# Performance work log

Hardware: AMD Instinct MI355X
Metric: run time of the kernel (lower is better)

The kernel has to match this reference:

```python
import jax, jax.numpy as jnp
import numpy as np
import math

B, S, H = 2, 2048, 2048
NH, NKV, HD = 16, 4, 128


def _rope_tables(seq_len, head_dim):
    # Standard RoPE: freqs over half dim, duplicated to full head_dim.
    inv_freq = 1.0 / (10000.0 ** (np.arange(0, head_dim, 2, dtype=np.float32) / head_dim))
    t = np.arange(seq_len, dtype=np.float32)
    freqs = np.outer(t, inv_freq)  # [S, HD/2]
    emb = np.concatenate([freqs, freqs], axis=-1)  # [S, HD]
    return jnp.asarray(np.cos(emb)), jnp.asarray(np.sin(emb))


def setup_inputs() -> dict:
    key = jax.random.key(0)
    k1, k2, k3, k4 = jax.random.split(key, 4)
    cos, sin = _rope_tables(S, HD)
    return {
        "x": jax.random.normal(k1, (B, S, H), dtype=jnp.float32),
        "cos": cos,
        "sin": sin,
        "Wq": jax.random.normal(k2, (H, NH * HD), dtype=jnp.float32) * (1.0 / math.sqrt(H)),
        "Wkv": jax.random.normal(k3, (H, 2 * NKV * HD), dtype=jnp.float32) * (1.0 / math.sqrt(H)),
        "Wo": jax.random.normal(k4, (NH * HD, H), dtype=jnp.float32) * (1.0 / math.sqrt(NH * HD)),
    }


def _rotate_half(x):
    x1, x2 = jnp.split(x, 2, axis=-1)
    return jnp.concatenate([-x2, x1], axis=-1)


def _apply_rotary(x, cos, sin):
    # x: [B, S, nheads, HD]; cos/sin: [S, HD]
    c = cos[None, :, None, :]
    s = sin[None, :, None, :]
    return x * c + _rotate_half(x) * s


def reference(x, cos, sin, Wq, Wkv, Wo):
    b, s, _ = x.shape
    q = (x @ Wq).reshape(b, s, NH, HD)
    kv = x @ Wkv
    k, v = jnp.split(kv, [NKV * HD], axis=-1)
    k = k.reshape(b, s, NKV, HD)
    v = v.reshape(b, s, NKV, HD)
    q = _apply_rotary(q, cos, sin)
    k = _apply_rotary(k, cos, sin)
    # to [B, heads, S, HD]
    q = jnp.transpose(q, (0, 2, 1, 3))
    k = jnp.transpose(k, (0, 2, 1, 3))
    v = jnp.transpose(v, (0, 2, 1, 3))
    # GQA: repeat K/V heads
    rep = NH // NKV
    k = jnp.repeat(k, rep, axis=1)
    v = jnp.repeat(v, rep, axis=1)
    scale = jnp.asarray(1.0 / math.sqrt(HD), dtype=x.dtype)
    scores = jnp.einsum('bhqd,bhkd->bhqk', q * scale, k)  # [B, NH, S, S]
    causal = jnp.tril(jnp.ones((s, s), dtype=jnp.bool_))
    scores = jnp.where(causal, scores, jnp.asarray(-jnp.inf, scores.dtype))
    attn = jax.nn.softmax(scores, axis=-1)
    out = jnp.einsum('bhqk,bhkd->bhqd', attn, v)
    out = jnp.transpose(out, (0, 2, 1, 3)).reshape(b, s, NH * HD)
    return out @ Wo
```

## Files before the change

### kernel.cpp

```cpp
#include <hip/hip_runtime.h>
#include <math.h>

#define NB 2
#define SEQ 2048
#define HDIM 2048
#define NHD 16
#define NKVH 4
#define HEADD 128
#define MROWS (NB*SEQ)
#define NQCOLS (NHD*HEADD)
#define QKVCOLS 3072

typedef unsigned short ushortT;
typedef __attribute__((ext_vector_type(8))) short short8;
typedef __attribute__((ext_vector_type(4))) float floatx4;
typedef __attribute__((ext_vector_type(4))) unsigned short ushort4v;

__device__ __forceinline__ ushortT f2bf(float f) {
  union { float f; unsigned int u; } v; v.f = f;
  unsigned int r = v.u + 0x7FFFu + ((v.u >> 16) & 1u);
  return (ushortT)(r >> 16);
}
__device__ __forceinline__ float bf2f(ushortT u) {
  union { unsigned int u; float f; } v; v.u = ((unsigned int)u) << 16;
  return v.f;
}

__device__ __forceinline__ void gload16(const ushortT* g, ushortT* l) {
  __builtin_amdgcn_global_load_lds(
      (const __attribute__((address_space(1))) void*)g,
      (__attribute__((address_space(3))) void*)l, 16, 0, 0);
}

__global__ __launch_bounds__(256) void cast_bf16_kernel(
    const float* __restrict__ in, ushortT* __restrict__ out, int n4) {
  int i = blockIdx.x * 256 + threadIdx.x;
  if (i >= n4) return;
  float4 v = ((const float4*)in)[i];
  ushort4v o;
  o.x = f2bf(v.x); o.y = f2bf(v.y); o.z = f2bf(v.z); o.w = f2bf(v.w);
  ((ushort4v*)out)[i] = o;
}

__global__ __launch_bounds__(256) void transpose_cast_kernel(
    const float* __restrict__ in, ushortT* __restrict__ out, int R, int C) {
  __shared__ ushortT tile[32][33];
  int c0 = blockIdx.x * 32, r0 = blockIdx.y * 32;
  int tx = threadIdx.x & 31, ty = threadIdx.x >> 5;
#pragma unroll
  for (int i = 0; i < 4; ++i)
    tile[ty + i*8][tx] = f2bf(in[(size_t)(r0 + ty + i*8) * C + c0 + tx]);
  __syncthreads();
#pragma unroll
  for (int i = 0; i < 4; ++i)
    out[(size_t)(c0 + ty + i*8) * R + r0 + tx] = tile[tx][ty + i*8];
}

__global__ __launch_bounds__(256) void gemm_bt_kernel(
    const ushortT* __restrict__ A, const ushortT* __restrict__ Bt,
    void* __restrict__ C, int M, int N, int K, int c_fp32) {
  __shared__ __align__(16) ushortT lA[128 * 64];
  __shared__ __align__(16) ushortT lB[128 * 64];
  const int m0 = blockIdx.y * 128;
  const int n0 = blockIdx.x * 128;
  const int tid = threadIdx.x;
  const int wave = tid >> 6, lane = tid & 63;
  const int g = lane >> 4, l15 = lane & 15;
  const int wm = (wave >> 1) * 64, wn = (wave & 1) * 64;
  const int sw = l15 & 7;

  floatx4 acc[4][4] = {};

  for (int kt = 0; kt < K; kt += 64) {
    __syncthreads();
#pragma unroll
    for (int i = 0; i < 4; ++i) {
      int s = i * 256 + tid;
      int r = s >> 3, j = s & 7;
      int col8 = j ^ (r & 7);
      gload16(A  + (size_t)(m0 + r) * K + kt + col8 * 8, lA + s * 8);
      gload16(Bt + (size_t)(n0 + r) * K + kt + col8 * 8, lB + s * 8);
    }
    __syncthreads();
#pragma unroll
    for (int ks = 0; ks < 2; ++ks) {
      short8 af[4], bfv[4];
#pragma unroll
      for (int t = 0; t < 4; ++t) {
        af[t]  = *(const short8*)(lA + (wm + t * 16 + l15) * 64 + ((ks * 4 + g) ^ sw) * 8);
        bfv[t] = *(const short8*)(lB + (wn + t * 16 + l15) * 64 + ((ks * 4 + g) ^ sw) * 8);
      }
#pragma unroll
      for (int mt = 0; mt < 4; ++mt)
#pragma unroll
        for (int nt = 0; nt < 4; ++nt)
          acc[mt][nt] = __builtin_amdgcn_mfma_f32_16x16x32_bf16(
              af[mt], bfv[nt], acc[mt][nt], 0, 0, 0);
    }
  }

#pragma unroll
  for (int mt = 0; mt < 4; ++mt)
#pragma unroll
    for (int nt = 0; nt < 4; ++nt)
#pragma unroll
      for (int r = 0; r < 4; ++r) {
        int row = m0 + wm + mt * 16 + g * 4 + r;
        int col = n0 + wn + nt * 16 + l15;
        float v = acc[mt][nt][r];
        if (c_fp32) ((float*)C)[(size_t)row * N + col] = v;
        else ((ushortT*)C)[(size_t)row * N + col] = f2bf(v);
      }
}

__global__ __launch_bounds__(256) void rope_q_kernel(
    const ushortT* __restrict__ QKVtmp, const float* __restrict__ cosT,
    const float* __restrict__ sinT, ushortT* __restrict__ Qr) {
  int idx = blockIdx.x * 256 + threadIdx.x;
  int d = idx & 63;
  int t = idx >> 6;
  int h = t & (NHD - 1);
  int bs = t >> 4;
  int s = bs & (SEQ - 1);
  int b = bs >> 11;
  float c = cosT[s * HEADD + d], sn = sinT[s * HEADD + d];
  float q1 = bf2f(QKVtmp[(size_t)bs * QKVCOLS + h * HEADD + d]);
  float q2 = bf2f(QKVtmp[(size_t)bs * QKVCOLS + h * HEADD + d + 64]);
  size_t o = ((size_t)(b * NHD + h) * SEQ + s) * HEADD + d;
  Qr[o]      = f2bf(q1 * c - q2 * sn);
  Qr[o + 64] = f2bf(q2 * c + q1 * sn);
}

__global__ __launch_bounds__(256) void rope_k_kernel(
    const ushortT* __restrict__ QKVtmp, const float* __restrict__ cosT,
    const float* __restrict__ sinT, ushortT* __restrict__ Kr) {
  int idx = blockIdx.x * 256 + threadIdx.x;
  int d = idx & 63;
  int t = idx >> 6;
  int kvh = t & (NKVH - 1);
  int bs = t >> 2;
  int s = bs & (SEQ - 1);
  int b = bs >> 11;
  float c = cosT[s * HEADD + d], sn = sinT[s * HEADD + d];
  float k1 = bf2f(QKVtmp[(size_t)bs * QKVCOLS + 2048 + kvh * HEADD + d]);
  float k2 = bf2f(QKVtmp[(size_t)bs * QKVCOLS + 2048 + kvh * HEADD + d + 64]);
  size_t o = ((size_t)(b * NKVH + kvh) * SEQ + s) * HEADD + d;
  Kr[o]      = f2bf(k1 * c - k2 * sn);
  Kr[o + 64] = f2bf(k2 * c + k1 * sn);
}

__global__ __launch_bounds__(256) void v_relayout_kernel(
    const ushortT* __restrict__ QKVtmp, ushortT* __restrict__ Vt) {
  __shared__ ushortT tile[32][33];
  int bk = blockIdx.z;
  int b = bk >> 2, kvh = bk & 3;
  int s0 = blockIdx.x * 32, d0 = blockIdx.y * 32;
  int tx = threadIdx.x & 31, ty = threadIdx.x >> 5;
#pragma unroll
  for (int i = 0; i < 4; ++i) {
    int s = s0 + ty + i * 8;
    tile[ty + i * 8][tx] =
        QKVtmp[(size_t)(b * SEQ + s) * QKVCOLS + 2560 + kvh * HEADD + d0 + tx];
  }
  __syncthreads();
#pragma unroll
  for (int i = 0; i < 4; ++i) {
    int d = d0 + ty + i * 8;
    Vt[((size_t)bk * HEADD + d) * SEQ + s0 + tx] = tile[tx][ty + i * 8];
  }
}

__global__ __launch_bounds__(256) void attn_kernel(
    const ushortT* __restrict__ Q,
    const ushortT* __restrict__ Kg,
    const ushortT* __restrict__ Vg,
    ushortT* __restrict__ Oa) {
  __shared__ __align__(16) ushortT lK[64 * 128];
  __shared__ __align__(16) ushortT lV[128 * 64];
  __shared__ __align__(16) ushortT lP[4 * 32 * 72];

  const int tid = threadIdx.x;
  const int w = tid >> 6, lane = tid & 63;
  const int g = lane >> 4, l15 = lane & 15;
  const int sw = l15 & 7;
  const int bh = blockIdx.x;
  const int b = bh >> 4, h = bh & 15;
  const int kvh = h >> 2;
  const int yi = blockIdx.y;
  const int qi = (yi < 8) ? (15 - yi) : (yi - 8);
  const int q0 = qi << 7;
  const int qw = q0 + w * 32;

  const float SC = 0.08838834764831845f * 1.4426950408889634f;

  short8 qf[2][4];
#pragma unroll
  for (int mt = 0; mt < 2; ++mt) {
    const ushortT* qp =
        Q + (((size_t)(b * NHD + h)) * SEQ + qw + mt * 16 + l15) * HEADD + g * 8;
#pragma unroll
    for (int ks = 0; ks < 4; ++ks) qf[mt][ks] = *(const short8*)(qp + ks * 32);
  }

  floatx4 o[2][8] = {};
  float m_s[2] = {-INFINITY, -INFINITY};
  float l_s[2] = {0.f, 0.f};

  const ushortT* kbase = Kg + ((size_t)(b * NKVH + kvh)) * SEQ * HEADD;
  const ushortT* vbase = Vg + ((size_t)(b * NKVH + kvh)) * HEADD * SEQ;
  ushortT* pw = lP + w * 32 * 72;

  const int nkt = 2 * qi + 2;
  for (int kt = 0; kt < nkt; ++kt) {
    __syncthreads();
#pragma unroll
    for (int ii = 0; ii < 4; ++ii) {
      int s = ii * 256 + tid;
      int r = s >> 4, j = (s & 15) ^ (r & 7);
      gload16(kbase + (size_t)(kt * 64 + r) * HEADD + j * 8, lK + s * 8);
    }
#pragma unroll
    for (int ii = 0; ii < 4; ++ii) {
      int s = ii * 256 + tid;
      int r = s >> 3, j = (s & 7) ^ (r & 7);
      gload16(vbase + (size_t)r * SEQ + kt * 64 + j * 8, lV + s * 8);
    }
    __syncthreads();

    if (kt == nkt - 1 && w < 2) continue;

    floatx4 sc[2][4] = {};
#pragma unroll
    for (int ks = 0; ks < 4; ++ks)
#pragma unroll
      for (int nt = 0; nt < 4; ++nt) {
        short8 kf = *(const short8*)(lK + (nt * 16 + l15) * 128 + ((ks * 4 + g) ^ sw) * 8);
        sc[0][nt] = __builtin_amdgcn_mfma_f32_16x16x32_bf16(kf, qf[0][ks], sc[0][nt], 0, 0, 0);
        sc[1][nt] = __builtin_amdgcn_mfma_f32_16x16x32_bf16(kf, qf[1][ks], sc[1][nt], 0, 0, 0);
      }

#pragma unroll
    for (int mt = 0; mt < 2; ++mt) {
      const int qsub = qw + mt * 16;
      const bool needmask = (kt * 64 + 63) > qsub;
      float ps[4][4];
      float mx = -INFINITY;
#pragma unroll
      for (int nt = 0; nt < 4; ++nt)
#pragma unroll
        for (int r = 0; r < 4; ++r) {
          float v = sc[mt][nt][r] * SC;
          if (needmask) {
            int kg = kt * 64 + nt * 16 + g * 4 + r;
            if (kg > qsub + l15) v = -INFINITY;
          }
          ps[nt][r] = v;
          mx = fmaxf(mx, v);
        }
      mx = fmaxf(mx, __shfl_xor(mx, 16));
      mx = fmaxf(mx, __shfl_xor(mx, 32));
      float mn = fmaxf(m_s[mt], mx);
      float alpha = __builtin_amdgcn_exp2f(m_s[mt] - mn);
      m_s[mt] = mn;
      float rs = 0.f;
#pragma unroll
      for (int nt = 0; nt < 4; ++nt) {
        ushort4v pk;
#pragma unroll
        for (int r = 0; r < 4; ++r) {
          float e = __builtin_amdgcn_exp2f(ps[nt][r] - mn);
          rs += e;
          ((ushortT*)&pk)[r] = f2bf(e);
        }
        *(ushort4v*)(pw + (mt * 16 + l15) * 72 + nt * 16 + g * 4) = pk;
      }
      rs += __shfl_xor(rs, 16);
      rs += __shfl_xor(rs, 32);
      l_s[mt] = l_s[mt] * alpha + rs;
#pragma unroll
      for (int dt = 0; dt < 8; ++dt)
#pragma unroll
        for (int r = 0; r < 4; ++r) o[mt][dt][r] *= alpha;
    }

#pragma unroll
    for (int ks = 0; ks < 2; ++ks) {
      short8 bp0 = *(const short8*)(pw + (0 * 16 + l15) * 72 + ks * 32 + g * 8);
      short8 bp1 = *(const short8*)(pw + (1 * 16 + l15) * 72 + ks * 32 + g * 8);
#pragma unroll
      for (int dt = 0; dt < 8; ++dt) {
        short8 vf = *(const short8*)(lV + (dt * 16 + l15) * 64 + ((ks * 4 + g) ^ sw) * 8);
        o[0][dt] = __builtin_amdgcn_mfma_f32_16x16x32_bf16(vf, bp0, o[0][dt], 0, 0, 0);
        o[1][dt] = __builtin_amdgcn_mfma_f32_16x16x32_bf16(vf, bp1, o[1][dt], 0, 0, 0);
      }
    }
  }

#pragma unroll
  for (int mt = 0; mt < 2; ++mt) {
    float inv = 1.f / l_s[mt];
    int qg = qw + mt * 16 + l15;
#pragma unroll
    for (int dt = 0; dt < 8; ++dt) {
      ushort4v ov;
#pragma unroll
      for (int r = 0; r < 4; ++r) ((ushortT*)&ov)[r] = f2bf(o[mt][dt][r] * inv);
      *(ushort4v*)(Oa + (size_t)(b * SEQ + qg) * NQCOLS + h * HEADD + dt * 16 + g * 4) = ov;
    }
  }
}

extern "C" void kernel_launch(void* const* d_in, const int* in_sizes, int n_in,
                              void* d_out, int out_size, void* d_ws, size_t ws_size,
                              hipStream_t stream) {
  const float* x    = (const float*)d_in[0];
  const float* cosT = (const float*)d_in[1];
  const float* sinT = (const float*)d_in[2];
  const float* Wq   = (const float*)d_in[3];
  const float* Wkv  = (const float*)d_in[4];
  const float* Wo   = (const float*)d_in[5];

  char* ws = (char*)d_ws;
  ushortT* x_bf   = (ushortT*)(ws + 0);
  ushortT* Wqkvt  = (ushortT*)(ws + 16777216);
  ushortT* Wot    = (ushortT*)(ws + 29360128);
  ushortT* QKVtmp = (ushortT*)(ws + 37748736);
  ushortT* Qr     = (ushortT*)(ws + 62914560);
  ushortT* Kr     = (ushortT*)(ws + 79691776);
  ushortT* Vt     = (ushortT*)(ws + 83886080);
  ushortT* Oattn  = QKVtmp;

  cast_bf16_kernel<<<8192, 256, 0, stream>>>(x, x_bf, (MROWS * HDIM) / 4);
  transpose_cast_kernel<<<dim3(64, 64), 256, 0, stream>>>(Wq, Wqkvt, HDIM, NQCOLS);
  transpose_cast_kernel<<<dim3(32, 64), 256, 0, stream>>>(Wkv, Wqkvt + 2048 * 2048, HDIM, 1024);
  transpose_cast_kernel<<<dim3(64, 64), 256, 0, stream>>>(Wo, Wot, NQCOLS, HDIM);

  gemm_bt_kernel<<<dim3(24, 32), 256, 0, stream>>>(x_bf, Wqkvt, QKVtmp, MROWS, QKVCOLS, HDIM, 0);

  rope_q_kernel<<<16384, 256, 0, stream>>>(QKVtmp, cosT, sinT, Qr);
  rope_k_kernel<<<4096, 256, 0, stream>>>(QKVtmp, cosT, sinT, Kr);
  v_relayout_kernel<<<dim3(64, 4, 8), 256, 0, stream>>>(QKVtmp, Vt);

  attn_kernel<<<dim3(32, 16), 256, 0, stream>>>(Qr, Kr, Vt, Oattn);

  gemm_bt_kernel<<<dim3(16, 32), 256, 0, stream>>>(Oattn, Wot, d_out, MROWS, HDIM, NQCOLS, 1);
}
```

Before: 374.1 us.

## Shrink attention query tile to 64 rows and skip fully masked MFMA subtiles

```diff
diff --git a/kernel.cpp b/kernel.cpp
--- a/kernel.cpp
+++ b/kernel.cpp
@@ -177,7 +177,7 @@
     ushortT* __restrict__ Oa) {
   __shared__ __align__(16) ushortT lK[64 * 128];
   __shared__ __align__(16) ushortT lV[128 * 64];
-  __shared__ __align__(16) ushortT lP[4 * 32 * 72];
+  __shared__ __align__(16) ushortT lP[4 * 16 * 72];
 
   const int tid = threadIdx.x;
   const int w = tid >> 6, lane = tid & 63;
@@ -186,31 +186,29 @@
   const int bh = blockIdx.x;
   const int b = bh >> 4, h = bh & 15;
   const int kvh = h >> 2;
-  const int yi = blockIdx.y;
-  const int qi = (yi < 8) ? (15 - yi) : (yi - 8);
-  const int q0 = qi << 7;
-  const int qw = q0 + w * 32;
+  const int qi = 31 - (int)blockIdx.y;
+  const int q0 = qi << 6;
+  const int qw = q0 + w * 16;
 
   const float SC = 0.08838834764831845f * 1.4426950408889634f;
 
-  short8 qf[2][4];
-#pragma unroll
-  for (int mt = 0; mt < 2; ++mt) {
+  short8 qf[4];
+  {
     const ushortT* qp =
-        Q + (((size_t)(b * NHD + h)) * SEQ + qw + mt * 16 + l15) * HEADD + g * 8;
-#pragma unroll
-    for (int ks = 0; ks < 4; ++ks) qf[mt][ks] = *(const short8*)(qp + ks * 32);
-  }
-
-  floatx4 o[2][8] = {};
-  float m_s[2] = {-INFINITY, -INFINITY};
-  float l_s[2] = {0.f, 0.f};
+        Q + (((size_t)(b * NHD + h)) * SEQ + qw + l15) * HEADD + g * 8;
+#pragma unroll
+    for (int ks = 0; ks < 4; ++ks) qf[ks] = *(const short8*)(qp + ks * 32);
+  }
+
+  floatx4 o[8] = {};
+  float m_s = -INFINITY;
+  float l_s = 0.f;
 
   const ushortT* kbase = Kg + ((size_t)(b * NKVH + kvh)) * SEQ * HEADD;
   const ushortT* vbase = Vg + ((size_t)(b * NKVH + kvh)) * HEADD * SEQ;
-  ushortT* pw = lP + w * 32 * 72;
-
-  const int nkt = 2 * qi + 2;
+  ushortT* pw = lP + w * 16 * 72;
+
+  const int nkt = qi + 1;
   for (int kt = 0; kt < nkt; ++kt) {
     __syncthreads();
 #pragma unroll
@@ -227,84 +225,83 @@
     }
     __syncthreads();
 
-    if (kt == nkt - 1 && w < 2) continue;
-
-    floatx4 sc[2][4] = {};
-#pragma unroll
-    for (int ks = 0; ks < 4; ++ks)
-#pragma unroll
-      for (int nt = 0; nt < 4; ++nt) {
+    const int rel = qw - kt * 64;
+
+    floatx4 sc[4] = {};
+    __builtin_amdgcn_s_setprio(1);
+#pragma unroll
+    for (int nt = 0; nt < 4; ++nt) {
+      if (nt * 16 > rel + 15) continue;
+#pragma unroll
+      for (int ks = 0; ks < 4; ++ks) {
         short8 kf = *(const short8*)(lK + (nt * 16 + l15) * 128 + ((ks * 4 + g) ^ sw) * 8);
-        sc[0][nt] = __builtin_amdgcn_mfma_f32_16x16x32_bf16(kf, qf[0][ks], sc[0][nt], 0, 0, 0);
-        sc[1][nt] = __builtin_amdgcn_mfma_f32_16x16x32_bf16(kf, qf[1][ks], sc[1][nt], 0, 0, 0);
-      }
-
-#pragma unroll
-    for (int mt = 0; mt < 2; ++mt) {
-      const int qsub = qw + mt * 16;
-      const bool needmask = (kt * 64 + 63) > qsub;
-      float ps[4][4];
-      float mx = -INFINITY;
-#pragma unroll
-      for (int nt = 0; nt < 4; ++nt)
-#pragma unroll
-        for (int r = 0; r < 4; ++r) {
-          float v = sc[mt][nt][r] * SC;
-          if (needmask) {
-            int kg = kt * 64 + nt * 16 + g * 4 + r;
-            if (kg > qsub + l15) v = -INFINITY;
-          }
-          ps[nt][r] = v;
-          mx = fmaxf(mx, v);
+        sc[nt] = __builtin_amdgcn_mfma_f32_16x16x32_bf16(kf, qf[ks], sc[nt], 0, 0, 0);
+      }
+    }
+    __builtin_amdgcn_s_setprio(0);
+
+    const bool needmask = (kt * 64 + 63) > qw;
+    float ps[4][4];
+    float mx = -INFINITY;
+#pragma unroll
+    for (int nt = 0; nt < 4; ++nt)
+#pragma unroll
+      for (int r = 0; r < 4; ++r) {
+        float v = sc[nt][r] * SC;
+        if (needmask) {
+          int kg = kt * 64 + nt * 16 + g * 4 + r;
+          if (kg > qw + l15) v = -INFINITY;
         }
-      mx = fmaxf(mx, __shfl_xor(mx, 16));
-      mx = fmaxf(mx, __shfl_xor(mx, 32));
-      float mn = fmaxf(m_s[mt], mx);
-      float alpha = __builtin_amdgcn_exp2f(m_s[mt] - mn);
-      m_s[mt] = mn;
-      float rs = 0.f;
-#pragma unroll
-      for (int nt = 0; nt < 4; ++nt) {
-        ushort4v pk;
-#pragma unroll
-        for (int r = 0; r < 4; ++r) {
-          float e = __builtin_amdgcn_exp2f(ps[nt][r] - mn);
-          rs += e;
-          ((ushortT*)&pk)[r] = f2bf(e);
-        }
-        *(ushort4v*)(pw + (mt * 16 + l15) * 72 + nt * 16 + g * 4) = pk;
-      }
-      rs += __shfl_xor(rs, 16);
-      rs += __shfl_xor(rs, 32);
-      l_s[mt] = l_s[mt] * alpha + rs;
-#pragma unroll
-      for (int dt = 0; dt < 8; ++dt)
-#pragma unroll
-        for (int r = 0; r < 4; ++r) o[mt][dt][r] *= alpha;
-    }
-
+        ps[nt][r] = v;
+        mx = fmaxf(mx, v);
+      }
+    mx = fmaxf(mx, __shfl_xor(mx, 16));
+    mx = fmaxf(mx, __shfl_xor(mx, 32));
+    float mn = fmaxf(m_s, mx);
+    float alpha = __builtin_amdgcn_exp2f(m_s - mn);
+    m_s = mn;
+    float rs = 0.f;
+#pragma unroll
+    for (int nt = 0; nt < 4; ++nt) {
+      ushort4v pk;
+#pragma unroll
+      for (int r = 0; r < 4; ++r) {
+        float e = __builtin_amdgcn_exp2f(ps[nt][r] - mn);
+        rs += e;
+        ((ushortT*)&pk)[r] = f2bf(e);
+      }
+      *(ushort4v*)(pw + l15 * 72 + nt * 16 + g * 4) = pk;
+    }
+    rs += __shfl_xor(rs, 16);
+    rs += __shfl_xor(rs, 32);
+    l_s = l_s * alpha + rs;
+#pragma unroll
+    for (int dt = 0; dt < 8; ++dt)
+#pragma unroll
+      for (int r = 0; r < 4; ++r) o[dt][r] *= alpha;
+
+    __builtin_amdgcn_s_setprio(1);
 #pragma unroll
     for (int ks = 0; ks < 2; ++ks) {
-      short8 bp0 = *(const short8*)(pw + (0 * 16 + l15) * 72 + ks * 32 + g * 8);
-      short8 bp1 = *(const short8*)(pw + (1 * 16 + l15) * 72 + ks * 32 + g * 8);
+      if (kt * 64 + ks * 32 > qw + 15) continue;
+      short8 bp = *(const short8*)(pw + l15 * 72 + ks * 32 + g * 8);
 #pragma unroll
       for (int dt = 0; dt < 8; ++dt) {
         short8 vf = *(const short8*)(lV + (dt * 16 + l15) * 64 + ((ks * 4 + g) ^ sw) * 8);
-        o[0][dt] = __builtin_amdgcn_mfma_f32_16x16x32_bf16(vf, bp0, o[0][dt], 0, 0, 0);
-        o[1][dt] = __builtin_amdgcn_mfma_f32_16x16x32_bf16(vf, bp1, o[1][dt], 0, 0, 0);
-      }
-    }
-  }
-
-#pragma unroll
-  for (int mt = 0; mt < 2; ++mt) {
-    float inv = 1.f / l_s[mt];
-    int qg = qw + mt * 16 + l15;
+        o[dt] = __builtin_amdgcn_mfma_f32_16x16x32_bf16(vf, bp, o[dt], 0, 0, 0);
+      }
+    }
+    __builtin_amdgcn_s_setprio(0);
+  }
+
+  {
+    float inv = 1.f / l_s;
+    int qg = qw + l15;
 #pragma unroll
     for (int dt = 0; dt < 8; ++dt) {
       ushort4v ov;
 #pragma unroll
-      for (int r = 0; r < 4; ++r) ((ushortT*)&ov)[r] = f2bf(o[mt][dt][r] * inv);
+      for (int r = 0; r < 4; ++r) ((ushortT*)&ov)[r] = f2bf(o[dt][r] * inv);
       *(ushort4v*)(Oa + (size_t)(b * SEQ + qg) * NQCOLS + h * HEADD + dt * 16 + g * 4) = ov;
     }
   }
@@ -341,7 +338,7 @@
   rope_k_kernel<<<4096, 256, 0, stream>>>(QKVtmp, cosT, sinT, Kr);
   v_relayout_kernel<<<dim3(64, 4, 8), 256, 0, stream>>>(QKVtmp, Vt);
 
-  attn_kernel<<<dim3(32, 16), 256, 0, stream>>>(Qr, Kr, Vt, Oattn);
+  attn_kernel<<<dim3(32, 32), 256, 0, stream>>>(Qr, Kr, Vt, Oattn);
 
   gemm_bt_kernel<<<dim3(16, 32), 256, 0, stream>>>(Oattn, Wot, d_out, MROWS, HDIM, NQCOLS, 1);
 }
```

Result: faster. 337.4 us (-9.8%).
